# Kernel optimization log

Hardware: AMD Instinct MI355X
Metric: run time of the kernel (lower is better)

Reference implementation:

```python
import jax, jax.numpy as jnp
import numpy as np

N_HEAD = 16
N_QUERY_GROUPS = 4
HEAD_SIZE = 64
ROPE_THETA = 10000.0


def apply_rope(x, theta=ROPE_THETA):
    # x: (B, H, T, D) -- lucidrains interleaved-pair rotary embedding
    B, H, T, D = x.shape
    inv_freq = 1.0 / (theta ** (jnp.arange(0, D, 2, dtype=jnp.float32) / D))  # (D/2,)
    freqs = jnp.arange(T, dtype=jnp.float32)[:, None] * inv_freq[None, :]      # (T, D/2)
    freqs = jnp.repeat(freqs, 2, axis=-1)                                      # (T, D)
    cos = jnp.cos(freqs).astype(x.dtype)
    sin = jnp.sin(freqs).astype(x.dtype)
    x1 = x[..., 0::2]
    x2 = x[..., 1::2]
    rot = jnp.stack((-x2, x1), axis=-1).reshape(x.shape)  # rotate_half, interleaved
    return x * cos + rot * sin


def setup_inputs() -> dict:
    key = jax.random.key(0)
    k1, k2, k3 = jax.random.split(key, 3)
    n_embd = N_HEAD * HEAD_SIZE
    qkv_dim = (N_HEAD + 2 * N_QUERY_GROUPS) * HEAD_SIZE
    x = jax.random.normal(k1, (1, 2048, n_embd), dtype=jnp.float32)
    w_attn = jax.random.normal(k2, (n_embd, qkv_dim), dtype=jnp.float32) * (n_embd ** -0.5)
    w_proj = jax.random.normal(k3, (n_embd, n_embd), dtype=jnp.float32) * (n_embd ** -0.5)
    return {"x": x, "w_attn": w_attn, "w_proj": w_proj}


def reference(x, w_attn, w_proj):
    B, T, C = x.shape
    q_per_kv = N_HEAD // N_QUERY_GROUPS
    total_qkv = q_per_kv + 2
    qkv = (x @ w_attn).reshape(B, T, N_QUERY_GROUPS, total_qkv, HEAD_SIZE)
    q = qkv[:, :, :, :q_per_kv, :].reshape(B, T, N_HEAD, HEAD_SIZE)
    k = qkv[:, :, :, q_per_kv:q_per_kv + 1, :].reshape(B, T, N_QUERY_GROUPS, HEAD_SIZE)
    v = qkv[:, :, :, q_per_kv + 1:, :].reshape(B, T, N_QUERY_GROUPS, HEAD_SIZE)
    # (B, H, T, D)
    q = q.transpose(0, 2, 1, 3)
    k = k.transpose(0, 2, 1, 3)
    v = v.transpose(0, 2, 1, 3)
    q = apply_rope(q)
    k = apply_rope(k)
    # GQA: broadcast each kv group to its q_per_kv query heads (repeat_interleave)
    k = jnp.repeat(k, q_per_kv, axis=1)
    v = jnp.repeat(v, q_per_kv, axis=1)
    scale = 1.0 / jnp.sqrt(jnp.asarray(HEAD_SIZE, dtype=q.dtype))
    att = jnp.einsum('bhqd,bhkd->bhqk', q, k) * scale
    causal = jnp.tril(jnp.ones((T, T), dtype=bool))
    att = jnp.where(causal, att, jnp.asarray(-jnp.inf, dtype=att.dtype))
    att = jax.nn.softmax(att, axis=-1)
    y = jnp.einsum('bhqk,bhkd->bhqd', att, v)
    y = y.transpose(0, 2, 1, 3).reshape(B, T, N_HEAD * HEAD_SIZE)
    return y @ w_proj
```

## Files before the change

kernel.cpp:

```cpp
#include <hip/hip_runtime.h>

#define T_SEQ 2048
#define C_EMB 1024
#define C_QKV 1536
#define N_HEAD 16

typedef __bf16 bf16x8 __attribute__((ext_vector_type(8)));
typedef __bf16 bf16x4 __attribute__((ext_vector_type(4)));
typedef float  f32x4  __attribute__((ext_vector_type(4)));

__device__ __forceinline__ void load_lds16(const __bf16* g, __bf16* l)
{
    __builtin_amdgcn_global_load_lds(
        (const __attribute__((address_space(1))) unsigned int*)g,
        (__attribute__((address_space(3))) unsigned int*)l, 16, 0, 0);
}

__device__ __forceinline__ void tconv_tile(
    const float* __restrict__ in, __bf16* __restrict__ out,
    int R, int C, int r0, int c0, float (*lds)[65], int t)
{
#pragma unroll
    for (int k = 0; k < 16; k++) {
        int r = k * 4 + (t >> 6), c = t & 63;
        lds[r][c] = in[(size_t)(r0 + r) * C + c0 + c];
    }
    __syncthreads();
#pragma unroll
    for (int k = 0; k < 16; k++) {
        int cc = k * 4 + (t >> 6), rr = t & 63;
        out[(size_t)(c0 + cc) * R + r0 + rr] = (__bf16)lds[rr][cc];
    }
}

__global__ __launch_bounds__(256) void prep_kernel(
    const float* __restrict__ x, const float* __restrict__ wa,
    const float* __restrict__ wp, __bf16* __restrict__ x_bf,
    __bf16* __restrict__ waT, __bf16* __restrict__ wpT)
{
    __shared__ float lds[64][65];
    const int b = blockIdx.x, t = threadIdx.x;
    if (b < 384) {
        tconv_tile(wa, waT, C_EMB, C_QKV, (b / 24) * 64, (b % 24) * 64, lds, t);
    } else if (b < 640) {
        int b2 = b - 384;
        tconv_tile(wp, wpT, C_EMB, C_EMB, (b2 / 16) * 64, (b2 % 16) * 64, lds, t);
    } else {
        for (int gi = (b - 640) * 256 + t; gi < T_SEQ * C_EMB / 8; gi += 65536) {
            float4 v0 = ((const float4*)x)[gi * 2];
            float4 v1 = ((const float4*)x)[gi * 2 + 1];
            bf16x8 o = { (__bf16)v0.x, (__bf16)v0.y, (__bf16)v0.z, (__bf16)v0.w,
                         (__bf16)v1.x, (__bf16)v1.y, (__bf16)v1.z, (__bf16)v1.w };
            ((bf16x8*)x_bf)[gi] = o;
        }
    }
}

template <bool FUSE_QKV>
__global__ __launch_bounds__(256) void gemm_mfma_kernel(
    const __bf16* __restrict__ A, const __bf16* __restrict__ Bt,
    __bf16* __restrict__ Cq, __bf16* __restrict__ Vt,
    float* __restrict__ Cf, int M, int N, int K)
{
    __shared__ __align__(16) __bf16 As0[64 * 64], As1[64 * 64];
    __shared__ __align__(16) __bf16 Bs0[64 * 64], Bs1[64 * 64];

    const int tid = threadIdx.x;
    const int l = tid & 63, w = tid >> 6;
    const int ln = l & 15, q = l >> 4;
    const int wm = (w & 1) * 32, wn = (w >> 1) * 32;
    const int row0 = blockIdx.y * 64, col0 = blockIdx.x * 64;

    f32x4 acc[2][2];
#pragma unroll
    for (int mi = 0; mi < 2; mi++)
#pragma unroll
        for (int ni = 0; ni < 2; ni++) acc[mi][ni] = (f32x4){0.f, 0.f, 0.f, 0.f};

    auto stage = [&](int k0, __bf16* as, __bf16* bs) {
#pragma unroll
        for (int p = 0; p < 2; p++) {
            int r = p * 32 + w * 8 + (l >> 3);
            int cc = (l & 7) ^ (r & 7);
            load_lds16(A + (size_t)(row0 + r) * K + k0 + cc * 8,
                       as + p * 2048 + w * 512);
            load_lds16(Bt + (size_t)(col0 + r) * K + k0 + cc * 8,
                       bs + p * 2048 + w * 512);
        }
    };
    auto compute = [&](const __bf16* as, const __bf16* bs) {
#pragma unroll
        for (int ki = 0; ki < 2; ki++) {
            bf16x8 af[2], bfr[2];
#pragma unroll
            for (int mi = 0; mi < 2; mi++)
                af[mi] = *(const bf16x8*)&as[(wm + mi * 16 + ln) * 64 +
                                             (((ki * 4 + q) ^ (ln & 7)) * 8)];
#pragma unroll
            for (int ni = 0; ni < 2; ni++)
                bfr[ni] = *(const bf16x8*)&bs[(wn + ni * 16 + ln) * 64 +
                                              (((ki * 4 + q) ^ (ln & 7)) * 8)];
#pragma unroll
            for (int mi = 0; mi < 2; mi++)
#pragma unroll
                for (int ni = 0; ni < 2; ni++)
                    acc[mi][ni] = __builtin_amdgcn_mfma_f32_16x16x32_bf16(
                        af[mi], bfr[ni], acc[mi][ni], 0, 0, 0);
        }
    };

    stage(0, As0, Bs0);
    for (int k0 = 0;; k0 += 128) {
        __syncthreads();
        if (k0 + 64 < K) stage(k0 + 64, As1, Bs1);
        compute(As0, Bs0);
        if (k0 + 64 >= K) break;
        __syncthreads();
        if (k0 + 128 < K) stage(k0 + 128, As0, Bs0);
        compute(As1, Bs1);
        if (k0 + 128 >= K) break;
    }

#pragma unroll
    for (int mi = 0; mi < 2; mi++)
#pragma unroll
        for (int ni = 0; ni < 2; ni++) {
            const int col = col0 + wn + ni * 16 + ln;
            if (!FUSE_QKV) {
#pragma unroll
                for (int reg = 0; reg < 4; reg++) {
                    int row = row0 + wm + mi * 16 + 4 * q + reg;
                    Cf[(size_t)row * N + col] = acc[mi][ni][reg];
                }
            } else {
                const int r = col % 384;
                const int gg = col / 384;
                if (r < 320) {
                    const int d = r & 63;
                    const float inv_freq =
                        __expf(-(float)(d & ~1) * (9.210340371976184f / 64.0f));
                    const float sgn = (d & 1) ? 1.0f : -1.0f;
                    const float osc = (r < 256) ? 0.18033688011112042f : 1.0f;
#pragma unroll
                    for (int reg = 0; reg < 4; reg++) {
                        int row = row0 + wm + mi * 16 + 4 * q + reg;
                        float v = acc[mi][ni][reg];
                        float pv = __shfl_xor(v, 1, 64);
                        float sn, cs;
                        sincosf((float)row * inv_freq, &sn, &cs);
                        Cq[(size_t)row * C_QKV + col] =
                            (__bf16)((v * cs + sgn * pv * sn) * osc);
                    }
                } else {
                    const int d = r - 320;
#pragma unroll
                    for (int reg = 0; reg < 4; reg++) {
                        int row = row0 + wm + mi * 16 + 4 * q + reg;
                        Vt[(size_t)(gg * 64 + d) * T_SEQ + row] =
                            (__bf16)acc[mi][ni][reg];
                    }
                }
            }
        }
}

__global__ __launch_bounds__(128) void attn_mfma_kernel(
    const __bf16* __restrict__ qkv, const __bf16* __restrict__ Vt,
    __bf16* __restrict__ y, __bf16* __restrict__ Opart,
    float* __restrict__ lpart)
{
    __shared__ __align__(16) __bf16 Ks0[64 * 64], Ks1[64 * 64];
    __shared__ __align__(16) __bf16 Vs0[64 * 64], Vs1[64 * 64];
    __shared__ __align__(16) __bf16 Ps[64 * 72];

    const int tid = threadIdx.x;
    const int l = tid & 63, w = tid >> 6;
    const int ln = l & 15, q = l >> 4;
    const int x = blockIdx.x, h = blockIdx.y;
    int qb, t0, t1;
    bool partial;
    if (x < 16)      { qb = 15 - x;  t0 = 0;             t1 = qb + 1;        partial = false; }
    else if (x < 32) { qb = x;       t0 = 0;             t1 = (qb + 2) >> 1; partial = true;  }
    else             { qb = x - 16;  t0 = (qb + 2) >> 1; t1 = qb + 1;        partial = true;  }

    const int g = h >> 2, hj = h & 3;
    const int qbase = g * 384 + hj * 64;
    const int kbase = g * 384 + 256;

    bf16x8 qa[2][2];
#pragma unroll
    for (int qj = 0; qj < 2; qj++) {
        const int qrow = qb * 64 + w * 32 + qj * 16 + ln;
#pragma unroll
        for (int ki = 0; ki < 2; ki++)
            qa[qj][ki] = *(const bf16x8*)(qkv + (size_t)qrow * C_QKV + qbase +
                                          ki * 32 + q * 8);
    }

    f32x4 O[2][4];
#pragma unroll
    for (int qj = 0; qj < 2; qj++)
#pragma unroll
        for (int ni = 0; ni < 4; ni++) O[qj][ni] = (f32x4){0.f, 0.f, 0.f, 0.f};
    float lsum[2] = {0.f, 0.f};

    auto stage = [&](int kt, __bf16* ks, __bf16* vs) {
#pragma unroll
        for (int p = 0; p < 4; p++) {
            int r = p * 16 + w * 8 + (l >> 3);
            int cc = (l & 7) ^ (r & 7);
            load_lds16(qkv + (size_t)(kt * 64 + r) * C_QKV + kbase + cc * 8,
                       ks + p * 1024 + w * 512);
            load_lds16(Vt + (size_t)(g * 64 + r) * T_SEQ + kt * 64 + cc * 8,
                       vs + p * 1024 + w * 512);
        }
    };
    auto compute = [&](int kt, const __bf16* ks, const __bf16* vs) {
        f32x4 s[2][4];
#pragma unroll
        for (int qj = 0; qj < 2; qj++)
#pragma unroll
            for (int ni = 0; ni < 4; ni++) s[qj][ni] = (f32x4){0.f, 0.f, 0.f, 0.f};
#pragma unroll
        for (int ki = 0; ki < 2; ki++)
#pragma unroll
            for (int ni = 0; ni < 4; ni++) {
                bf16x8 kb = *(const bf16x8*)&ks[(ni * 16 + ln) * 64 +
                                                (((ki * 4 + q) ^ (ln & 7)) * 8)];
#pragma unroll
                for (int qj = 0; qj < 2; qj++)
                    s[qj][ni] = __builtin_amdgcn_mfma_f32_16x16x32_bf16(
                        kb, qa[qj][ki], s[qj][ni], 0, 0, 0);
            }

        const bool diag = (kt == qb);
#pragma unroll
        for (int qj = 0; qj < 2; qj++)
#pragma unroll
            for (int ni = 0; ni < 4; ni++) {
                bf16x4 pp;
#pragma unroll
                for (int reg = 0; reg < 4; reg++) {
                    float v = s[qj][ni][reg];
                    if (diag && (ni * 16 + 4 * q + reg) > (w * 32 + qj * 16 + ln))
                        v = -1e30f;
                    float p = exp2f(v);
                    lsum[qj] += p;
                    pp[reg] = (__bf16)p;
                }
                *(bf16x4*)&Ps[(w * 32 + qj * 16 + ln) * 72 + ni * 16 + 4 * q] = pp;
            }

#pragma unroll
        for (int ki = 0; ki < 2; ki++) {
            bf16x8 pa[2];
#pragma unroll
            for (int qj = 0; qj < 2; qj++)
                pa[qj] = *(const bf16x8*)&Ps[(w * 32 + qj * 16 + ln) * 72 +
                                             ki * 32 + q * 8];
#pragma unroll
            for (int ni = 0; ni < 4; ni++) {
                bf16x8 vb = *(const bf16x8*)&vs[(ni * 16 + ln) * 64 +
                                                (((ki * 4 + q) ^ (ln & 7)) * 8)];
#pragma unroll
                for (int qj = 0; qj < 2; qj++)
                    O[qj][ni] = __builtin_amdgcn_mfma_f32_16x16x32_bf16(
                        vb, pa[qj], O[qj][ni], 0, 0, 0);
            }
        }
    };

    stage(t0, Ks0, Vs0);
    for (int kt = t0;;) {
        __syncthreads();
        if (kt + 1 < t1) stage(kt + 1, Ks1, Vs1);
        compute(kt, Ks0, Vs0);
        if (++kt >= t1) break;
        __syncthreads();
        if (kt + 1 < t1) stage(kt + 1, Ks0, Vs0);
        compute(kt, Ks1, Vs1);
        if (++kt >= t1) break;
    }

#pragma unroll
    for (int qj = 0; qj < 2; qj++) {
        float ls = lsum[qj];
        ls += __shfl_xor(ls, 16, 64);
        ls += __shfl_xor(ls, 32, 64);
        const int t = qb * 64 + w * 32 + qj * 16 + ln;

        if (!partial) {
            const float inv = 1.0f / ls;
#pragma unroll
            for (int ni = 0; ni < 4; ni++) {
                bf16x4 o;
#pragma unroll
                for (int reg = 0; reg < 4; reg++) o[reg] = (__bf16)(O[qj][ni][reg] * inv);
                *(bf16x4*)&y[(size_t)t * C_EMB + h * 64 + ni * 16 + 4 * q] = o;
            }
        } else {
            const int half = (x >= 32);
            const int tr = t - 1024;
            __bf16* od = Opart + (size_t)half * 1024 * C_EMB +
                         (size_t)tr * C_EMB + h * 64;
            if (q == 0) lpart[half * 16 * 1024 + h * 1024 + tr] = ls;
#pragma unroll
            for (int ni = 0; ni < 4; ni++) {
                bf16x4 o;
#pragma unroll
                for (int reg = 0; reg < 4; reg++) o[reg] = (__bf16)O[qj][ni][reg];
                *(bf16x4*)&od[ni * 16 + 4 * q] = o;
            }
        }
    }
}

__global__ __launch_bounds__(256) void merge_kernel(
    const __bf16* __restrict__ Opart, const float* __restrict__ lpart,
    __bf16* __restrict__ y)
{
    const size_t base = ((size_t)blockIdx.x * 256 + threadIdx.x) * 8;
    const int tr = (int)(base >> 10);
    const int c = (int)(base & 1023);
    const int h = c >> 6;
    const float inv = 1.0f / (lpart[h * 1024 + tr] +
                              lpart[16 * 1024 + h * 1024 + tr]);
    bf16x8 a = *(const bf16x8*)&Opart[base];
    bf16x8 b = *(const bf16x8*)&Opart[(size_t)1024 * C_EMB + base];
    bf16x8 o;
#pragma unroll
    for (int i = 0; i < 8; i++)
        o[i] = (__bf16)(((float)a[i] + (float)b[i]) * inv);
    *(bf16x8*)&y[(size_t)(1024 + tr) * C_EMB + c] = o;
}

extern "C" void kernel_launch(void* const* d_in, const int* in_sizes, int n_in,
                              void* d_out, int out_size, void* d_ws, size_t ws_size,
                              hipStream_t stream)
{
    const float* x      = (const float*)d_in[0];
    const float* w_attn = (const float*)d_in[1];
    const float* w_proj = (const float*)d_in[2];
    float* out = (float*)d_out;

    __bf16* x_bf = (__bf16*)d_ws;
    __bf16* waT  = x_bf + (size_t)T_SEQ * C_EMB;
    __bf16* wpT  = waT  + (size_t)C_QKV * C_EMB;
    __bf16* qkv  = wpT  + (size_t)C_EMB * C_EMB;
    __bf16* Vt   = qkv  + (size_t)T_SEQ * C_QKV;
    __bf16* y_bf = Vt   + (size_t)256 * T_SEQ;
    __bf16* Opart = x_bf;
    float*  lpart = (float*)waT;

    prep_kernel<<<896, 256, 0, stream>>>(x, w_attn, w_proj, x_bf, waT, wpT);

    gemm_mfma_kernel<true><<<dim3(C_QKV / 64, T_SEQ / 64), 256, 0, stream>>>(
        x_bf, waT, qkv, Vt, nullptr, T_SEQ, C_QKV, C_EMB);

    attn_mfma_kernel<<<dim3(48, N_HEAD), 128, 0, stream>>>(
        qkv, Vt, y_bf, Opart, lpart);

    merge_kernel<<<512, 256, 0, stream>>>(Opart, lpart, y_bf);

    gemm_mfma_kernel<false><<<dim3(C_EMB / 64, T_SEQ / 64), 256, 0, stream>>>(
        y_bf, wpT, nullptr, nullptr, out, T_SEQ, C_EMB, C_EMB);
}
```

Measured before the change: 129.2 us.

## Use 128-row query tiles and split every query block's KV range in two

```diff
diff --git a/kernel.cpp b/kernel.cpp
--- a/kernel.cpp
+++ b/kernel.cpp
@@ -164,24 +164,26 @@
         }
 }
 
-__global__ __launch_bounds__(128) void attn_mfma_kernel(
+__global__ __launch_bounds__(256) void attn_mfma_kernel(
     const __bf16* __restrict__ qkv, const __bf16* __restrict__ Vt,
     __bf16* __restrict__ y, __bf16* __restrict__ Opart,
     float* __restrict__ lpart)
 {
     __shared__ __align__(16) __bf16 Ks0[64 * 64], Ks1[64 * 64];
     __shared__ __align__(16) __bf16 Vs0[64 * 64], Vs1[64 * 64];
-    __shared__ __align__(16) __bf16 Ps[64 * 72];
+    __shared__ __align__(16) __bf16 Ps[128 * 72];
 
     const int tid = threadIdx.x;
     const int l = tid & 63, w = tid >> 6;
     const int ln = l & 15, q = l >> 4;
-    const int x = blockIdx.x, h = blockIdx.y;
-    int qb, t0, t1;
-    bool partial;
-    if (x < 16)      { qb = 15 - x;  t0 = 0;             t1 = qb + 1;        partial = false; }
-    else if (x < 32) { qb = x;       t0 = 0;             t1 = (qb + 2) >> 1; partial = true;  }
-    else             { qb = x - 16;  t0 = (qb + 2) >> 1; t1 = qb + 1;        partial = true;  }
+
+    const int b = blockIdx.x;
+    const int rep = b >> 8, u = b & 255;
+    const int h = u & 15, s0 = u >> 4;
+    const int qb = rep ? (15 - s0) : s0;
+    const int t0 = rep ? (qb + 1) : 0;
+    const int t1 = rep ? (2 * qb + 2) : (qb + 1);
+    const int qb2 = qb * 2;
 
     const int g = h >> 2, hj = h & 3;
     const int qbase = g * 384 + hj * 64;
@@ -190,7 +192,7 @@
     bf16x8 qa[2][2];
 #pragma unroll
     for (int qj = 0; qj < 2; qj++) {
-        const int qrow = qb * 64 + w * 32 + qj * 16 + ln;
+        const int qrow = qb * 128 + w * 32 + qj * 16 + ln;
 #pragma unroll
         for (int ki = 0; ki < 2; ki++)
             qa[qj][ki] = *(const bf16x8*)(qkv + (size_t)qrow * C_QKV + qbase +
@@ -206,21 +208,21 @@
 
     auto stage = [&](int kt, __bf16* ks, __bf16* vs) {
 #pragma unroll
-        for (int p = 0; p < 4; p++) {
-            int r = p * 16 + w * 8 + (l >> 3);
+        for (int p = 0; p < 2; p++) {
+            int r = p * 32 + w * 8 + (l >> 3);
             int cc = (l & 7) ^ (r & 7);
             load_lds16(qkv + (size_t)(kt * 64 + r) * C_QKV + kbase + cc * 8,
-                       ks + p * 1024 + w * 512);
+                       ks + p * 2048 + w * 512);
             load_lds16(Vt + (size_t)(g * 64 + r) * T_SEQ + kt * 64 + cc * 8,
-                       vs + p * 1024 + w * 512);
+                       vs + p * 2048 + w * 512);
         }
     };
     auto compute = [&](int kt, const __bf16* ks, const __bf16* vs) {
-        f32x4 s[2][4];
+        f32x4 sc[2][4];
 #pragma unroll
         for (int qj = 0; qj < 2; qj++)
 #pragma unroll
-            for (int ni = 0; ni < 4; ni++) s[qj][ni] = (f32x4){0.f, 0.f, 0.f, 0.f};
+            for (int ni = 0; ni < 4; ni++) sc[qj][ni] = (f32x4){0.f, 0.f, 0.f, 0.f};
 #pragma unroll
         for (int ki = 0; ki < 2; ki++)
 #pragma unroll
@@ -229,27 +231,30 @@
                                                 (((ki * 4 + q) ^ (ln & 7)) * 8)];
 #pragma unroll
                 for (int qj = 0; qj < 2; qj++)
-                    s[qj][ni] = __builtin_amdgcn_mfma_f32_16x16x32_bf16(
-                        kb, qa[qj][ki], s[qj][ni], 0, 0, 0);
+                    sc[qj][ni] = __builtin_amdgcn_mfma_f32_16x16x32_bf16(
+                        kb, qa[qj][ki], sc[qj][ni], 0, 0, 0);
             }
 
-        const bool diag = (kt == qb);
-#pragma unroll
-        for (int qj = 0; qj < 2; qj++)
+        const int rel = kt - qb2;
+        const int koff = rel * 64;
+#pragma unroll
+        for (int qj = 0; qj < 2; qj++) {
+            const int qr = w * 32 + qj * 16 + ln;
 #pragma unroll
             for (int ni = 0; ni < 4; ni++) {
                 bf16x4 pp;
 #pragma unroll
                 for (int reg = 0; reg < 4; reg++) {
-                    float v = s[qj][ni][reg];
-                    if (diag && (ni * 16 + 4 * q + reg) > (w * 32 + qj * 16 + ln))
+                    float v = sc[qj][ni][reg];
+                    if (rel >= 0 && (koff + ni * 16 + 4 * q + reg) > qr)
                         v = -1e30f;
                     float p = exp2f(v);
                     lsum[qj] += p;
                     pp[reg] = (__bf16)p;
                 }
-                *(bf16x4*)&Ps[(w * 32 + qj * 16 + ln) * 72 + ni * 16 + 4 * q] = pp;
+                *(bf16x4*)&Ps[(qr)*72 + ni * 16 + 4 * q] = pp;
             }
+        }
 
 #pragma unroll
         for (int ki = 0; ki < 2; ki++) {
@@ -287,30 +292,15 @@
         float ls = lsum[qj];
         ls += __shfl_xor(ls, 16, 64);
         ls += __shfl_xor(ls, 32, 64);
-        const int t = qb * 64 + w * 32 + qj * 16 + ln;
-
-        if (!partial) {
-            const float inv = 1.0f / ls;
-#pragma unroll
-            for (int ni = 0; ni < 4; ni++) {
-                bf16x4 o;
-#pragma unroll
-                for (int reg = 0; reg < 4; reg++) o[reg] = (__bf16)(O[qj][ni][reg] * inv);
-                *(bf16x4*)&y[(size_t)t * C_EMB + h * 64 + ni * 16 + 4 * q] = o;
-            }
-        } else {
-            const int half = (x >= 32);
-            const int tr = t - 1024;
-            __bf16* od = Opart + (size_t)half * 1024 * C_EMB +
-                         (size_t)tr * C_EMB + h * 64;
-            if (q == 0) lpart[half * 16 * 1024 + h * 1024 + tr] = ls;
-#pragma unroll
-            for (int ni = 0; ni < 4; ni++) {
-                bf16x4 o;
-#pragma unroll
-                for (int reg = 0; reg < 4; reg++) o[reg] = (__bf16)O[qj][ni][reg];
-                *(bf16x4*)&od[ni * 16 + 4 * q] = o;
-            }
+        const int t = qb * 128 + w * 32 + qj * 16 + ln;
+        __bf16* od = (rep ? Opart : y) + (size_t)t * C_EMB + h * 64;
+        if (q == 0) lpart[rep * 16 * 2048 + h * 2048 + t] = ls;
+#pragma unroll
+        for (int ni = 0; ni < 4; ni++) {
+            bf16x4 o;
+#pragma unroll
+            for (int reg = 0; reg < 4; reg++) o[reg] = (__bf16)O[qj][ni][reg];
+            *(bf16x4*)&od[ni * 16 + 4 * q] = o;
         }
     }
 }
@@ -320,18 +310,18 @@
     __bf16* __restrict__ y)
 {
     const size_t base = ((size_t)blockIdx.x * 256 + threadIdx.x) * 8;
-    const int tr = (int)(base >> 10);
+    const int t = (int)(base >> 10);
     const int c = (int)(base & 1023);
     const int h = c >> 6;
-    const float inv = 1.0f / (lpart[h * 1024 + tr] +
-                              lpart[16 * 1024 + h * 1024 + tr]);
-    bf16x8 a = *(const bf16x8*)&Opart[base];
-    bf16x8 b = *(const bf16x8*)&Opart[(size_t)1024 * C_EMB + base];
+    const float inv = 1.0f / (lpart[h * 2048 + t] +
+                              lpart[16 * 2048 + h * 2048 + t]);
+    bf16x8 a = *(const bf16x8*)&y[base];
+    bf16x8 bb = *(const bf16x8*)&Opart[base];
     bf16x8 o;
 #pragma unroll
     for (int i = 0; i < 8; i++)
-        o[i] = (__bf16)(((float)a[i] + (float)b[i]) * inv);
-    *(bf16x8*)&y[(size_t)(1024 + tr) * C_EMB + c] = o;
+        o[i] = (__bf16)(((float)a[i] + (float)bb[i]) * inv);
+    *(bf16x8*)&y[base] = o;
 }
 
 extern "C" void kernel_launch(void* const* d_in, const int* in_sizes, int n_in,
@@ -357,10 +347,10 @@
     gemm_mfma_kernel<true><<<dim3(C_QKV / 64, T_SEQ / 64), 256, 0, stream>>>(
         x_bf, waT, qkv, Vt, nullptr, T_SEQ, C_QKV, C_EMB);
 
-    attn_mfma_kernel<<<dim3(48, N_HEAD), 128, 0, stream>>>(
+    attn_mfma_kernel<<<512, 256, 0, stream>>>(
         qkv, Vt, y_bf, Opart, lpart);
 
-    merge_kernel<<<512, 256, 0, stream>>>(Opart, lpart, y_bf);
+    merge_kernel<<<1024, 256, 0, stream>>>(Opart, lpart, y_bf);
 
     gemm_mfma_kernel<false><<<dim3(C_EMB / 64, T_SEQ / 64), 256, 0, stream>>>(
         y_bf, wpT, nullptr, nullptr, out, T_SEQ, C_EMB, C_EMB);
```

New measurement: 128.7 us. About the same (-0.4%).
